# Optimization experiments

Hardware: AMD Instinct MI355X
Metric: run time of the kernel (lower is better)

Reference implementation:

```python
import jax, jax.numpy as jnp
import numpy as np

# ---- static hash-grid config (matches tcnn HashGrid in __init__) ----
L = 16            # n_levels
T = 1 << 19       # hashmap size per level
BASE = 16
MAXR = 4096
GEO = 15
SCALE = np.exp((np.log(MAXR) - np.log(BASE)) / (L - 1))
RES = np.floor(BASE * SCALE ** np.arange(L)).astype(np.int64)  # per-level resolution
PRIMES = np.array([1, 2654435761, 805459861], dtype=np.uint32)
CORNERS = np.array([[(i >> 2) & 1, (i >> 1) & 1, i & 1] for i in range(8)], dtype=np.float32)  # [8,3]


@jax.custom_vjp
def trunc_exp(x):
    return jnp.exp(x)

def _te_fwd(x):
    return jnp.exp(x), x

def _te_bwd(x, g):
    return (g * jnp.exp(jnp.minimum(x, 15.0)),)

trunc_exp.defvjp(_te_fwd, _te_bwd)


def hash_encode(x, tables):
    """Multi-res hash grid. x: [N,3] in [0,1]; tables: [L,T,2] -> [N, 2*L]."""
    x = jnp.clip(x, 0.0, 1.0)
    feats = []
    for l in range(L):  # fixed small loop over levels
        res = float(RES[l])
        pos = x * res                      # [N,3]
        p0 = jnp.floor(pos)
        f = pos - p0                       # trilinear fractions
        idx = (p0[:, None, :] + CORNERS[None]).astype(jnp.uint32)  # [N,8,3]
        h = (idx[..., 0] * PRIMES[0]) ^ (idx[..., 1] * PRIMES[1]) ^ (idx[..., 2] * PRIMES[2])
        h = (h % np.uint32(T)).astype(jnp.int32)                   # [N,8]
        w = jnp.prod(jnp.where(CORNERS[None] > 0, f[:, None, :], 1.0 - f[:, None, :]), axis=-1)  # [N,8]
        feats.append(jnp.sum(tables[l][h] * w[..., None], axis=1))  # [N,2]
    return jnp.concatenate(feats, axis=-1)  # [N,32]


def sh_deg4(d):
    """Spherical harmonics degree 4 (16 comps) on unit directions d: [N,3]."""
    x, y, z = d[..., 0], d[..., 1], d[..., 2]
    x2, y2, z2 = x * x, y * y, z * z
    xy, yz, xz = x * y, y * z, x * z
    return jnp.stack([
        jnp.full_like(x, 0.28209479177387814),
        -0.48860251190291987 * y, 0.48860251190291987 * z, -0.48860251190291987 * x,
        1.0925484305920792 * xy, -1.0925484305920792 * yz,
        0.94617469575755997 * z2 - 0.31539156525252005,
        -1.0925484305920792 * xz, 0.54627421529603959 * (x2 - y2),
        -0.5900435899266435 * y * (3 * x2 - y2), 2.890611442640554 * xy * z,
        -0.4570457994644658 * y * (4 * z2 - x2 - y2),
        0.3731763325901154 * z * (2 * z2 - 3 * x2 - 3 * y2),
        -0.4570457994644658 * x * (4 * z2 - x2 - y2),
        1.445305721320277 * z * (x2 - y2),
        -0.5900435899266435 * x * (x2 - 3 * y2),
    ], axis=-1)


def setup_inputs() -> dict:
    key = jax.random.key(0)
    ks = jax.random.split(key, 12)
    R, N = 8192, 524288
    rays_o = jax.random.uniform(ks[0], (R, 3), minval=-0.4, maxval=0.4, dtype=jnp.float32)
    d = jax.random.normal(ks[1], (R, 3), dtype=jnp.float32)
    rays_d = d / jnp.linalg.norm(d, axis=-1, keepdims=True)
    ray_indices = jnp.sort(jax.random.randint(ks[2], (N,), 0, R)).astype(jnp.int32)
    t_starts = jax.random.uniform(ks[3], (N,), dtype=jnp.float32) * 0.25
    t_ends = t_starts + jax.random.uniform(ks[4], (N,), dtype=jnp.float32) * 0.02 + 1e-3
    hash_tables = jax.random.uniform(ks[5], (L, T, 2), minval=-1e-4, maxval=1e-4, dtype=jnp.float32)
    base_w0 = jax.random.normal(ks[6], (32, 64), dtype=jnp.float32) * (1.0 / np.sqrt(32))
    base_w1 = jax.random.normal(ks[7], (64, 16), dtype=jnp.float32) * (1.0 / np.sqrt(64))
    head_w0 = jax.random.normal(ks[8], (31, 64), dtype=jnp.float32) * (1.0 / np.sqrt(31))
    head_w1 = jax.random.normal(ks[9], (64, 64), dtype=jnp.float32) * (1.0 / np.sqrt(64))
    head_w2 = jax.random.normal(ks[10], (64, 3), dtype=jnp.float32) * (1.0 / np.sqrt(64))
    aabb = jnp.array([-1., -1., -1., 1., 1., 1.], dtype=jnp.float32)
    return dict(t_starts=t_starts, t_ends=t_ends, rays_o=rays_o, rays_d=rays_d,
                ray_indices=ray_indices, hash_tables=hash_tables,
                base_w0=base_w0, base_w1=base_w1,
                head_w0=head_w0, head_w1=head_w1, head_w2=head_w2, aabb=aabb)


def reference(t_starts, t_ends, rays_o, rays_d, ray_indices, hash_tables,
              base_w0, base_w1, head_w0, head_w1, head_w2, aabb):
    n_rays = rays_o.shape[0]
    aabb_min, aabb_max = aabb[:3], aabb[3:]
    # gather per-sample origins/dirs (irregular gather)
    t_origins = rays_o[ray_indices]
    t_dirs = rays_d[ray_indices]
    tmid = (t_starts + t_ends) * 0.5
    positions = t_origins + t_dirs * tmid[:, None]
    # query_density
    xn = (positions - aabb_min) / (aabb_max - aabb_min + 1e-5)
    selector = jnp.all((xn > 0.0) & (xn < 1.0), axis=-1)
    enc = hash_encode(xn, hash_tables)                   # [N,32]
    h = jax.nn.relu(enc @ base_w0) @ base_w1             # [N,16]
    sigmas = trunc_exp(h[:, 0] - 1.0) * selector         # [N]
    embedding = h[:, 1:]                                 # [N,15]
    # query_rgb: dir=(dir+1)/2 then SH enc maps back to [-1,1] => SH(t_dirs)
    hh = jnp.concatenate([sh_deg4(t_dirs), embedding], axis=-1)  # [N,31]
    rgbs = jax.nn.sigmoid(jax.nn.relu(jax.nn.relu(hh @ head_w0) @ head_w1) @ head_w2)  # [N,3]
    # render_weight_from_density: segment-wise exclusive transmittance
    s = sigmas * (t_ends - t_starts)
    excl = jnp.cumsum(s) - s                              # global exclusive cumsum
    offsets = jax.ops.segment_min(excl, ray_indices, num_segments=n_rays)  # value at each segment start
    trans = jnp.exp(-(excl - offsets[ray_indices]))
    alphas = 1.0 - jnp.exp(-s)
    weights = trans * alphas
    # accumulate_along_rays (segment_sum scatter)
    colors = jax.ops.segment_sum(weights[:, None] * rgbs, ray_indices, num_segments=n_rays)
    opacities = jax.ops.segment_sum(weights, ray_indices, num_segments=n_rays)[:, None]
    depths = jax.ops.segment_sum(weights * tmid, ray_indices, num_segments=n_rays)[:, None]
    depths = depths / jnp.maximum(opacities, jnp.finfo(jnp.float32).eps)  # expected_depths
    return colors, opacities, depths
```

## Files before the change

kernel.cpp:

```cpp
#include <hip/hip_runtime.h>
#include <math.h>

#define NLEV 16
#define TBL  (1u << 19)
#define TMASK (TBL - 1u)

typedef _Float16 half2v  __attribute__((ext_vector_type(2)));
typedef _Float16 half4   __attribute__((ext_vector_type(4)));
typedef _Float16 half8   __attribute__((ext_vector_type(8)));
typedef float    floatx4 __attribute__((ext_vector_type(4)));
typedef unsigned int uint2v __attribute__((ext_vector_type(2)));
typedef unsigned int uint4v __attribute__((ext_vector_type(4)));

struct ResParams { float resf[NLEV]; };

__device__ __forceinline__ float sigmoidf(float x) {
    return 1.0f / (1.0f + __expf(-x));
}

__device__ __forceinline__ float2 unpack_h2(unsigned u) {
    union { unsigned u; half2v h; } c; c.u = u;
    return make_float2((float)c.h[0], (float)c.h[1]);
}

__device__ __forceinline__ int swz64(int row, int col) {
    return row * 64 + ((((col >> 3) ^ (row & 7)) << 3) | (col & 7));
}
__device__ __forceinline__ int swz64_blk(int row, int blk) {
    return row * 64 + ((blk ^ (row & 7)) << 3);
}
__device__ __forceinline__ int swz16(int row, int col) {
    return row * 64 + ((((col >> 3) ^ (row & 7)) << 3) | (col & 7));
}
__device__ __forceinline__ int swz16_blk(int row, int blk) {
    return row * 64 + ((blk ^ (row & 7)) << 3);
}

__global__ __launch_bounds__(256) void k_cvt(
    const float* __restrict__ src, _Float16* __restrict__ dst, int n4)
{
    const int i = blockIdx.x * 256 + threadIdx.x;
    if (i >= n4) return;
    const float4 v = ((const float4*)src)[i];
    half4 o; o[0] = (_Float16)v.x; o[1] = (_Float16)v.y;
    o[2] = (_Float16)v.z; o[3] = (_Float16)v.w;
    ((half4*)dst)[i] = o;
}

struct SampPos { float x0, x1, x2; };

__device__ __forceinline__ SampPos load_pos(
    int i, const float* __restrict__ t_starts, const float* __restrict__ t_ends,
    const float* __restrict__ rays_o, const float* __restrict__ rays_d,
    const int* __restrict__ ray_indices,
    float a0, float a1, float a2, float ib0, float ib1, float ib2)
{
    const int   ri = ray_indices[i];
    const float tmid = 0.5f * (t_starts[i] + t_ends[i]);
    const float xn0 = (rays_o[ri*3+0] + rays_d[ri*3+0]*tmid - a0) * ib0;
    const float xn1 = (rays_o[ri*3+1] + rays_d[ri*3+1]*tmid - a1) * ib1;
    const float xn2 = (rays_o[ri*3+2] + rays_d[ri*3+2]*tmid - a2) * ib2;
    SampPos p;
    p.x0 = fminf(fmaxf(xn0, 0.f), 1.f);
    p.x1 = fminf(fmaxf(xn1, 0.f), 1.f);
    p.x2 = fminf(fmaxf(xn2, 0.f), 1.f);
    return p;
}

__global__ __launch_bounds__(256) void k_hash1(
    const float* __restrict__ t_starts, const float* __restrict__ t_ends,
    const float* __restrict__ rays_o,   const float* __restrict__ rays_d,
    const int*   __restrict__ ray_indices,
    const _Float16* __restrict__ tabh,
    const float* __restrict__ aabb,
    _Float16* __restrict__ encG, int n, ResParams rp)
{
    const int i = blockIdx.x * 256 + threadIdx.x;
    if (i >= n) return;

    const float a0 = aabb[0], a1 = aabb[1], a2 = aabb[2];
    const float ib0 = 1.f / (aabb[3] - a0 + 1e-5f);
    const float ib1 = 1.f / (aabb[4] - a1 + 1e-5f);
    const float ib2 = 1.f / (aabb[5] - a2 + 1e-5f);

    const SampPos A = load_pos(i, t_starts, t_ends, rays_o, rays_d, ray_indices,
                               a0, a1, a2, ib0, ib1, ib2);

    union { _Float16 h[32]; uint4v q[4]; } ev;

    #pragma unroll
    for (int l = 0; l < NLEV; ++l) {
        const float resf = rp.resf[l];
        const _Float16* __restrict__ tab = tabh + (size_t)l * (size_t)(TBL * 2u);

        const float p0 = A.x0*resf, p1 = A.x1*resf, p2 = A.x2*resf;
        const float fl0 = floorf(p0), fl1 = floorf(p1), fl2 = floorf(p2);
        const float f0 = p0-fl0, f1 = p1-fl1, f2 = p2-fl2;
        const unsigned i0 = (unsigned)fl0, i1 = (unsigned)fl1, i2 = (unsigned)fl2;
        const unsigned hy0 = i1 * 2654435761u, hy1 = hy0 + 2654435761u;
        const unsigned hz0 = i2 * 805459861u,  hz1 = hz0 + 805459861u;
        const float g0 = 1.f-f0, g1 = 1.f-f1, g2 = 1.f-f2;
        const unsigned ryz[4] = { hy0^hz0, hy0^hz1, hy1^hz0, hy1^hz1 };
        const float    wyz[4] = { g1*g2,   g1*f2,   f1*g2,   f1*f2 };

        unsigned v0[4], v1[4];
        if (!(i0 & 1u)) {
            #pragma unroll
            for (int c = 0; c < 4; ++c) {
                const unsigned lo = (i0 ^ ryz[c]) & TMASK;
                const uint2v p = *(const uint2v*)(tab + (size_t)(lo & ~1u) * 2u);
                const unsigned sw = lo & 1u;
                v0[c] = sw ? p.y : p.x;
                v1[c] = sw ? p.x : p.y;
            }
        } else {
            #pragma unroll
            for (int c = 0; c < 4; ++c) {
                const unsigned lo = (i0        ^ ryz[c]) & TMASK;
                const unsigned hi = ((i0 + 1u) ^ ryz[c]) & TMASK;
                v0[c] = *(const unsigned*)(tab + (size_t)lo * 2u);
                v1[c] = *(const unsigned*)(tab + (size_t)hi * 2u);
            }
        }

        float e0 = 0.f, e1 = 0.f;
        #pragma unroll
        for (int c = 0; c < 4; ++c) {
            const float wlo = g0 * wyz[c], whi = f0 * wyz[c];
            const float2 t0 = unpack_h2(v0[c]), t1 = unpack_h2(v1[c]);
            e0 += wlo * t0.x + whi * t1.x;
            e1 += wlo * t0.y + whi * t1.y;
        }
        ev.h[2*l]   = (_Float16)(e0 * 1024.f);
        ev.h[2*l+1] = (_Float16)(e1 * 1024.f);
    }

    uint4v* dst = (uint4v*)(encG + (size_t)i * 32);
    #pragma unroll
    for (int q = 0; q < 4; ++q) __builtin_nontemporal_store(ev.q[q], dst + q);
}

__global__ __launch_bounds__(256) void k_mlp(
    const float* __restrict__ t_starts, const float* __restrict__ t_ends,
    const float* __restrict__ rays_o,   const float* __restrict__ rays_d,
    const int*   __restrict__ ray_indices,
    const float* __restrict__ bw0,
    const float* __restrict__ bw1,
    const float* __restrict__ hw0,
    const float* __restrict__ hw1,
    const float* __restrict__ hw2,
    const float* __restrict__ aabb,
    const _Float16* __restrict__ encG,
    float4* __restrict__ srgb, int n)
{
    __shared__ _Float16 sT  [4][16 * 72];
    __shared__ _Float16 sSH [256 * 16];
    __shared__ _Float16 sHB [256 * 16];
    __shared__ _Float16 sW0T[64 * 40];
    __shared__ _Float16 sW1T[64 * 64];
    __shared__ _Float16 sBW0T[64 * 32];
    __shared__ _Float16 sBW1T[16 * 64];
    __shared__ float    sDT [256];

    const int t     = threadIdx.x;
    const int gbase = blockIdx.x * 256;

    {
        const int s  = gbase + t;
        const int ri = ray_indices[s];
        const float ts = t_starts[s], te = t_ends[s];
        const float tmid = 0.5f * (ts + te);
        const float ox = rays_o[ri*3+0], oy = rays_o[ri*3+1], oz = rays_o[ri*3+2];
        const float dx = rays_d[ri*3+0], dy = rays_d[ri*3+1], dz = rays_d[ri*3+2];
        const float a0 = aabb[0], a1 = aabb[1], a2c = aabb[2];
        const float b0 = aabb[3], b1 = aabb[4], b2c = aabb[5];
        const float xn0 = (ox + dx*tmid - a0) / (b0 - a0 + 1e-5f);
        const float xn1 = (oy + dy*tmid - a1) / (b1 - a1 + 1e-5f);
        const float xn2 = (oz + dz*tmid - a2c) / (b2c - a2c + 1e-5f);
        const bool sel = (xn0 > 0.f) && (xn0 < 1.f) && (xn1 > 0.f) && (xn1 < 1.f)
                      && (xn2 > 0.f) && (xn2 < 1.f);
        sDT[t] = sel ? (te - ts) : 0.f;

        const float x = dx, y = dy, z = dz;
        const float x2 = x*x, y2 = y*y, z2 = z*z;
        const float xy = x*y, yz = y*z, xz = x*z;
        float shv[16];
        shv[0]  = 0.28209479177387814f;
        shv[1]  = -0.48860251190291987f * y;
        shv[2]  = 0.48860251190291987f * z;
        shv[3]  = -0.48860251190291987f * x;
        shv[4]  = 1.0925484305920792f * xy;
        shv[5]  = -1.0925484305920792f * yz;
        shv[6]  = 0.94617469575756f * z2 - 0.31539156525252005f;
        shv[7]  = -1.0925484305920792f * xz;
        shv[8]  = 0.5462742152960396f * (x2 - y2);
        shv[9]  = -0.5900435899266435f * y * (3.f*x2 - y2);
        shv[10] = 2.890611442640554f * xy * z;
        shv[11] = -0.4570457994644658f * y * (4.f*z2 - x2 - y2);
        shv[12] = 0.3731763325901154f * z * (2.f*z2 - 3.f*x2 - 3.f*y2);
        shv[13] = -0.4570457994644658f * x * (4.f*z2 - x2 - y2);
        shv[14] = 1.445305721320277f * z * (x2 - y2);
        shv[15] = -0.5900435899266435f * x * (x2 - 3.f*y2);
        #pragma unroll
        for (int k4 = 0; k4 < 4; ++k4) {
            half4 p;
            #pragma unroll
            for (int j = 0; j < 4; ++j) p[j] = (_Float16)shv[k4*4 + j];
            *(half4*)&sSH[t*16 + k4*4] = p;
        }
    }
    {
        const int nidx = t & 63, g = t >> 6;
        #pragma unroll
        for (int i2 = 0; i2 < 8; ++i2) {
            const int k = g*8 + i2;
            const float v = (k < 31) ? hw0[k*64 + nidx] : 0.f;
            sW0T[nidx*40 + k] = (_Float16)v;
        }
        #pragma unroll
        for (int i2 = 0; i2 < 16; ++i2) {
            const int k = g*16 + i2;
            sW1T[swz64(nidx, k)] = (_Float16)hw1[k*64 + nidx];
        }
        #pragma unroll
        for (int i2 = 0; i2 < 8; ++i2) {
            const int k = g*8 + i2;
            sBW0T[nidx*32 + k] = (_Float16)bw0[k*64 + nidx];
        }
    }
    {
        const int nidx = t & 15, g = t >> 4;
        #pragma unroll
        for (int i2 = 0; i2 < 4; ++i2) {
            const int k = g*4 + i2;
            sBW1T[swz16(nidx, k)] = (_Float16)bw1[k*16 + nidx];
        }
    }

    const int lane = t & 63, w = t >> 6;
    const int nn = lane & 15, quad = lane >> 4;
    _Float16* myT = &sT[w][0];

    half8 BH2[2];
    #pragma unroll
    for (int ks = 0; ks < 2; ++ks)
        #pragma unroll
        for (int j = 0; j < 8; ++j) {
            const int k = ks*32 + quad*8 + j;
            BH2[ks][j] = (nn < 3) ? (_Float16)hw2[k*3 + nn] : (_Float16)0.f;
        }

    __syncthreads();

    const int rbase = w * 64;

    #pragma unroll
    for (int rt = 0; rt < 4; ++rt) {
        const int srow = rbase + rt*16;
        const int drow = srow + quad*4;

        half8 bE = *(const half8*)(encG + (size_t)(gbase + srow + nn)*32 + quad*8);
        #pragma unroll
        for (int ct = 0; ct < 4; ++ct) {
            half8 aW = *(const half8*)&sBW0T[(ct*16 + nn)*32 + quad*8];
            floatx4 acc = {0.f, 0.f, 0.f, 0.f};
            acc = __builtin_amdgcn_mfma_f32_16x16x32_f16(aW, bE, acc, 0, 0, 0);
            half4 p;
            #pragma unroll
            for (int r2 = 0; r2 < 4; ++r2) p[r2] = (_Float16)fmaxf(acc[r2], 0.f);
            *(half4*)&myT[nn*72 + ct*16 + quad*4] = p;
        }

        float sigr[4];
        {
            half8 a20 = *(const half8*)&myT[nn*72 +  0 + quad*8];
            half8 a21 = *(const half8*)&myT[nn*72 + 32 + quad*8];
            half8 b20 = *(const half8*)&sBW1T[swz16_blk(nn, quad)];
            half8 b21 = *(const half8*)&sBW1T[swz16_blk(nn, 4 + quad)];
            floatx4 acc = {0.f, 0.f, 0.f, 0.f};
            acc = __builtin_amdgcn_mfma_f32_16x16x32_f16(a20, b20, acc, 0, 0, 0);
            acc = __builtin_amdgcn_mfma_f32_16x16x32_f16(a21, b21, acc, 0, 0, 0);
            #pragma unroll
            for (int r2 = 0; r2 < 4; ++r2) {
                const float h = acc[r2] * (1.f / 1024.f);
                const float h0 = __shfl(h, lane & 0x30, 64);
                sigr[r2] = __expf(h0 - 1.f) * sDT[drow + r2];
                if (nn == 0) sHB[(drow + r2)*16 + 15] = (_Float16)0.f;
                else         sHB[(drow + r2)*16 + (nn - 1)] = (_Float16)h;
            }
        }

        half8 shf = *(const half8*)&sSH[(srow + nn)*16 + (quad & 1)*8];
        half8 hbf = *(const half8*)&sHB[(srow + nn)*16 + (quad & 1)*8];
        half8 a3f = (quad < 2) ? shf : hbf;
        #pragma unroll
        for (int ct = 0; ct < 4; ++ct) {
            half8 aW = *(const half8*)&sW0T[(ct*16 + nn)*40 + quad*8];
            floatx4 acc = {0.f, 0.f, 0.f, 0.f};
            acc = __builtin_amdgcn_mfma_f32_16x16x32_f16(aW, a3f, acc, 0, 0, 0);
            half4 p;
            #pragma unroll
            for (int r2 = 0; r2 < 4; ++r2) p[r2] = (_Float16)fmaxf(acc[r2], 0.f);
            *(half4*)&myT[nn*72 + ct*16 + quad*4] = p;
        }

        half8 af0 = *(const half8*)&myT[nn*72 +  0 + quad*8];
        half8 af1 = *(const half8*)&myT[nn*72 + 32 + quad*8];
        #pragma unroll
        for (int ct = 0; ct < 4; ++ct) {
            half8 aW0 = *(const half8*)&sW1T[swz64_blk(ct*16 + nn, quad)];
            half8 aW1 = *(const half8*)&sW1T[swz64_blk(ct*16 + nn, 4 + quad)];
            floatx4 acc = {0.f, 0.f, 0.f, 0.f};
            acc = __builtin_amdgcn_mfma_f32_16x16x32_f16(aW0, af0, acc, 0, 0, 0);
            acc = __builtin_amdgcn_mfma_f32_16x16x32_f16(aW1, af1, acc, 0, 0, 0);
            half4 p;
            #pragma unroll
            for (int r2 = 0; r2 < 4; ++r2) p[r2] = (_Float16)fmaxf(acc[r2], 0.f);
            *(half4*)&myT[nn*72 + ct*16 + quad*4] = p;
        }

        {
            half8 a50 = *(const half8*)&myT[nn*72 +  0 + quad*8];
            half8 a51 = *(const half8*)&myT[nn*72 + 32 + quad*8];
            floatx4 acc = {0.f, 0.f, 0.f, 0.f};
            acc = __builtin_amdgcn_mfma_f32_16x16x32_f16(a50, BH2[0], acc, 0, 0, 0);
            acc = __builtin_amdgcn_mfma_f32_16x16x32_f16(a51, BH2[1], acc, 0, 0, 0);
            #pragma unroll
            for (int r2 = 0; r2 < 4; ++r2) {
                float* bp = (float*)&srgb[gbase + drow + r2];
                if (nn < 3)       bp[1 + nn] = sigmoidf(acc[r2]);
                else if (nn == 3) bp[0]      = sigr[r2];
            }
        }
    }
}

__global__ __launch_bounds__(256) void k_render(
    const float* __restrict__ t_starts, const float* __restrict__ t_ends,
    const int*   __restrict__ ray_indices,
    const float4* __restrict__ srgb,
    float* __restrict__ out, int n_samples, int n_rays)
{
    const int wid  = (blockIdx.x * 256 + threadIdx.x) >> 6;
    const int lane = threadIdx.x & 63;
    if (wid >= n_rays) return;
    const int r = wid;

    int lo = 0, hi = n_samples;
    while (lo < hi) { int mid = (lo + hi) >> 1; if (ray_indices[mid] <  r) lo = mid + 1; else hi = mid; }
    const int start = lo;
    hi = n_samples;
    while (lo < hi) { int mid = (lo + hi) >> 1; if (ray_indices[mid] <= r) lo = mid + 1; else hi = mid; }
    const int end = lo;

    float S = 0.f, cr = 0.f, cg = 0.f, cb = 0.f, op = 0.f, dw = 0.f;
    for (int j0 = start; j0 < end; j0 += 64) {
        const int j = j0 + lane;
        float s = 0.f, R = 0.f, G = 0.f, B = 0.f, tm = 0.f;
        if (j < end) {
            const float4 v = srgb[j];
            s = v.x; R = v.y; G = v.z; B = v.w;
            tm = 0.5f * (t_starts[j] + t_ends[j]);
        }
        float incl = s;
        #pragma unroll
        for (int off = 1; off < 64; off <<= 1) {
            const float tv = __shfl_up(incl, off, 64);
            if (lane >= off) incl += tv;
        }
        const float excl  = incl - s;
        const float trans = __expf(-(S + excl));
        const float alpha = 1.f - __expf(-s);
        const float wgt   = trans * alpha;
        cr += wgt * R; cg += wgt * G; cb += wgt * B;
        op += wgt;     dw += wgt * tm;
        S += __shfl(incl, 63, 64);
    }
    #pragma unroll
    for (int off = 1; off < 64; off <<= 1) {
        cr += __shfl_xor(cr, off, 64);
        cg += __shfl_xor(cg, off, 64);
        cb += __shfl_xor(cb, off, 64);
        op += __shfl_xor(op, off, 64);
        dw += __shfl_xor(dw, off, 64);
    }
    if (lane == 0) {
        out[r*3 + 0] = cr;
        out[r*3 + 1] = cg;
        out[r*3 + 2] = cb;
        out[n_rays*3 + r] = op;
        out[n_rays*4 + r] = dw / fmaxf(op, 1.1920929e-7f);
    }
}

extern "C" void kernel_launch(void* const* d_in, const int* in_sizes, int n_in,
                              void* d_out, int out_size, void* d_ws, size_t ws_size,
                              hipStream_t stream)
{
    const float* t_starts    = (const float*)d_in[0];
    const float* t_ends      = (const float*)d_in[1];
    const float* rays_o      = (const float*)d_in[2];
    const float* rays_d      = (const float*)d_in[3];
    const int*   ray_indices = (const int*)  d_in[4];
    const float* tables      = (const float*)d_in[5];
    const float* bw0         = (const float*)d_in[6];
    const float* bw1         = (const float*)d_in[7];
    const float* hw0         = (const float*)d_in[8];
    const float* hw1         = (const float*)d_in[9];
    const float* hw2         = (const float*)d_in[10];
    const float* aabb        = (const float*)d_in[11];

    const int n      = in_sizes[0];
    const int n_rays = in_sizes[2] / 3;
    const int tbl_n  = in_sizes[5];

    float* out = (float*)d_out;
    char*  ws  = (char*)d_ws;

    const size_t tabh_bytes = (size_t)tbl_n * 2;
    const size_t enc_bytes  = (size_t)n * 64;

    ResParams rp;
    const double scale = exp((log(4096.0) - log(16.0)) / 15.0);
    for (int l = 0; l < NLEV; ++l)
        rp.resf[l] = (float)floor(16.0 * pow(scale, (double)l));

    _Float16* tabh = (_Float16*)ws;
    _Float16* encG = (_Float16*)(ws + tabh_bytes);
    float4*   srgb = (float4*)(ws + tabh_bytes + enc_bytes);

    const int n4 = tbl_n / 4;
    k_cvt<<<(n4 + 255)/256, 256, 0, stream>>>(tables, tabh, n4);

    k_hash1<<<(n + 255)/256, 256, 0, stream>>>(
        t_starts, t_ends, rays_o, rays_d, ray_indices, tabh, aabb, encG, n, rp);

    k_mlp<<<(n + 255)/256, 256, 0, stream>>>(
        t_starts, t_ends, rays_o, rays_d, ray_indices, bw0, bw1, hw0, hw1, hw2,
        aabb, encG, srgb, n);
    k_render<<<(n_rays*64 + 255)/256, 256, 0, stream>>>(
        t_starts, t_ends, ray_indices, srgb, out, n, n_rays);
}
```

Measured before the change: 322.0 us.

## Interleave two MLP row tiles per wave and precompute ray segment bounds

The MLP kernel now processes two 16-row tiles at once, interleaving independent MFMA chains, and stores intermediate activations in a swizzled shared-memory layout instead of padded rows. The intent is to hide MFMA latency and reduce LDS bank conflicts. A new k_bounds kernel, preceded by a memset, records each ray's start and end sample index so the render kernel no longer runs two binary searches per ray. This adds an extra launch and memset, more registers per wave, and an extra workspace buffer placed after srgb.

```diff
diff --git a/kernel.cpp b/kernel.cpp
--- a/kernel.cpp
+++ b/kernel.cpp
@@ -138,6 +138,16 @@
     uint4v* dst = (uint4v*)(encG + (size_t)i * 32);
     #pragma unroll
     for (int q = 0; q < 4; ++q) __builtin_nontemporal_store(ev.q[q], dst + q);
+}
+
+__global__ __launch_bounds__(256) void k_bounds(
+    const int* __restrict__ ray_indices, int* __restrict__ se, int n)
+{
+    const int i = blockIdx.x * 256 + threadIdx.x;
+    if (i >= n) return;
+    const int r = ray_indices[i];
+    if (i == 0 || ray_indices[i-1] != r) se[2*r]     = i;
+    if (i == n-1 || ray_indices[i+1] != r) se[2*r+1] = i + 1;
 }
 
 __global__ __launch_bounds__(256) void k_mlp(
@@ -153,7 +163,7 @@
     const _Float16* __restrict__ encG,
     float4* __restrict__ srgb, int n)
 {
-    __shared__ _Float16 sT  [4][16 * 72];
+    __shared__ _Float16 sT  [4][2048];
     __shared__ _Float16 sSH [256 * 16];
     __shared__ _Float16 sHB [256 * 16];
     __shared__ _Float16 sW0T[64 * 40];
@@ -239,7 +249,8 @@
 
     const int lane = t & 63, w = t >> 6;
     const int nn = lane & 15, quad = lane >> 4;
-    _Float16* myT = &sT[w][0];
+    _Float16* T0 = &sT[w][0];
+    _Float16* T1 = &sT[w][1024];
 
     half8 BH2[2];
     #pragma unroll
@@ -255,81 +266,127 @@
     const int rbase = w * 64;
 
     #pragma unroll
-    for (int rt = 0; rt < 4; ++rt) {
-        const int srow = rbase + rt*16;
-        const int drow = srow + quad*4;
-
-        half8 bE = *(const half8*)(encG + (size_t)(gbase + srow + nn)*32 + quad*8);
+    for (int p = 0; p < 2; ++p) {
+        const int s0 = rbase + p*32;
+        const int s1 = s0 + 16;
+        const int d0 = s0 + quad*4;
+        const int d1 = s1 + quad*4;
+
+        half8 bE0 = *(const half8*)(encG + (size_t)(gbase + s0 + nn)*32 + quad*8);
+        half8 bE1 = *(const half8*)(encG + (size_t)(gbase + s1 + nn)*32 + quad*8);
         #pragma unroll
         for (int ct = 0; ct < 4; ++ct) {
             half8 aW = *(const half8*)&sBW0T[(ct*16 + nn)*32 + quad*8];
-            floatx4 acc = {0.f, 0.f, 0.f, 0.f};
-            acc = __builtin_amdgcn_mfma_f32_16x16x32_f16(aW, bE, acc, 0, 0, 0);
-            half4 p;
-            #pragma unroll
-            for (int r2 = 0; r2 < 4; ++r2) p[r2] = (_Float16)fmaxf(acc[r2], 0.f);
-            *(half4*)&myT[nn*72 + ct*16 + quad*4] = p;
-        }
-
-        float sigr[4];
+            floatx4 a0 = {0.f,0.f,0.f,0.f}, a1 = {0.f,0.f,0.f,0.f};
+            a0 = __builtin_amdgcn_mfma_f32_16x16x32_f16(aW, bE0, a0, 0, 0, 0);
+            a1 = __builtin_amdgcn_mfma_f32_16x16x32_f16(aW, bE1, a1, 0, 0, 0);
+            half4 p0, p1;
+            #pragma unroll
+            for (int r2 = 0; r2 < 4; ++r2) {
+                p0[r2] = (_Float16)fmaxf(a0[r2], 0.f);
+                p1[r2] = (_Float16)fmaxf(a1[r2], 0.f);
+            }
+            *(half4*)&T0[swz16(nn, ct*16 + quad*4)] = p0;
+            *(half4*)&T1[swz16(nn, ct*16 + quad*4)] = p1;
+        }
+
+        float sig0[4], sig1[4];
         {
-            half8 a20 = *(const half8*)&myT[nn*72 +  0 + quad*8];
-            half8 a21 = *(const half8*)&myT[nn*72 + 32 + quad*8];
             half8 b20 = *(const half8*)&sBW1T[swz16_blk(nn, quad)];
             half8 b21 = *(const half8*)&sBW1T[swz16_blk(nn, 4 + quad)];
-            floatx4 acc = {0.f, 0.f, 0.f, 0.f};
-            acc = __builtin_amdgcn_mfma_f32_16x16x32_f16(a20, b20, acc, 0, 0, 0);
-            acc = __builtin_amdgcn_mfma_f32_16x16x32_f16(a21, b21, acc, 0, 0, 0);
+            half8 a200 = *(const half8*)&T0[swz16_blk(nn, quad)];
+            half8 a201 = *(const half8*)&T0[swz16_blk(nn, 4 + quad)];
+            half8 a210 = *(const half8*)&T1[swz16_blk(nn, quad)];
+            half8 a211 = *(const half8*)&T1[swz16_blk(nn, 4 + quad)];
+            floatx4 c0 = {0.f,0.f,0.f,0.f}, c1 = {0.f,0.f,0.f,0.f};
+            c0 = __builtin_amdgcn_mfma_f32_16x16x32_f16(a200, b20, c0, 0, 0, 0);
+            c1 = __builtin_amdgcn_mfma_f32_16x16x32_f16(a210, b20, c1, 0, 0, 0);
+            c0 = __builtin_amdgcn_mfma_f32_16x16x32_f16(a201, b21, c0, 0, 0, 0);
+            c1 = __builtin_amdgcn_mfma_f32_16x16x32_f16(a211, b21, c1, 0, 0, 0);
             #pragma unroll
             for (int r2 = 0; r2 < 4; ++r2) {
-                const float h = acc[r2] * (1.f / 1024.f);
-                const float h0 = __shfl(h, lane & 0x30, 64);
-                sigr[r2] = __expf(h0 - 1.f) * sDT[drow + r2];
-                if (nn == 0) sHB[(drow + r2)*16 + 15] = (_Float16)0.f;
-                else         sHB[(drow + r2)*16 + (nn - 1)] = (_Float16)h;
-            }
-        }
-
-        half8 shf = *(const half8*)&sSH[(srow + nn)*16 + (quad & 1)*8];
-        half8 hbf = *(const half8*)&sHB[(srow + nn)*16 + (quad & 1)*8];
-        half8 a3f = (quad < 2) ? shf : hbf;
+                const float h0v = c0[r2] * (1.f / 1024.f);
+                const float h1v = c1[r2] * (1.f / 1024.f);
+                const float b0v = __shfl(h0v, lane & 0x30, 64);
+                const float b1v = __shfl(h1v, lane & 0x30, 64);
+                sig0[r2] = __expf(b0v - 1.f) * sDT[d0 + r2];
+                sig1[r2] = __expf(b1v - 1.f) * sDT[d1 + r2];
+                if (nn == 0) {
+                    sHB[(d0 + r2)*16 + 15] = (_Float16)0.f;
+                    sHB[(d1 + r2)*16 + 15] = (_Float16)0.f;
+                } else {
+                    sHB[(d0 + r2)*16 + (nn - 1)] = (_Float16)h0v;
+                    sHB[(d1 + r2)*16 + (nn - 1)] = (_Float16)h1v;
+                }
+            }
+        }
+
+        half8 sh0 = *(const half8*)&sSH[(s0 + nn)*16 + (quad & 1)*8];
+        half8 hb0 = *(const half8*)&sHB[(s0 + nn)*16 + (quad & 1)*8];
+        half8 sh1 = *(const half8*)&sSH[(s1 + nn)*16 + (quad & 1)*8];
+        half8 hb1 = *(const half8*)&sHB[(s1 + nn)*16 + (quad & 1)*8];
+        half8 f30 = (quad < 2) ? sh0 : hb0;
+        half8 f31 = (quad < 2) ? sh1 : hb1;
         #pragma unroll
         for (int ct = 0; ct < 4; ++ct) {
             half8 aW = *(const half8*)&sW0T[(ct*16 + nn)*40 + quad*8];
-            floatx4 acc = {0.f, 0.f, 0.f, 0.f};
-            acc = __builtin_amdgcn_mfma_f32_16x16x32_f16(aW, a3f, acc, 0, 0, 0);
-            half4 p;
-            #pragma unroll
-            for (int r2 = 0; r2 < 4; ++r2) p[r2] = (_Float16)fmaxf(acc[r2], 0.f);
-            *(half4*)&myT[nn*72 + ct*16 + quad*4] = p;
-        }
-
-        half8 af0 = *(const half8*)&myT[nn*72 +  0 + quad*8];
-        half8 af1 = *(const half8*)&myT[nn*72 + 32 + quad*8];
+            floatx4 a0 = {0.f,0.f,0.f,0.f}, a1 = {0.f,0.f,0.f,0.f};
+            a0 = __builtin_amdgcn_mfma_f32_16x16x32_f16(aW, f30, a0, 0, 0, 0);
+            a1 = __builtin_amdgcn_mfma_f32_16x16x32_f16(aW, f31, a1, 0, 0, 0);
+            half4 p0, p1;
+            #pragma unroll
+            for (int r2 = 0; r2 < 4; ++r2) {
+                p0[r2] = (_Float16)fmaxf(a0[r2], 0.f);
+                p1[r2] = (_Float16)fmaxf(a1[r2], 0.f);
+            }
+            *(half4*)&T0[swz16(nn, ct*16 + quad*4)] = p0;
+            *(half4*)&T1[swz16(nn, ct*16 + quad*4)] = p1;
+        }
+
+        half8 af00 = *(const half8*)&T0[swz16_blk(nn, quad)];
+        half8 af01 = *(const half8*)&T0[swz16_blk(nn, 4 + quad)];
+        half8 af10 = *(const half8*)&T1[swz16_blk(nn, quad)];
+        half8 af11 = *(const half8*)&T1[swz16_blk(nn, 4 + quad)];
         #pragma unroll
         for (int ct = 0; ct < 4; ++ct) {
             half8 aW0 = *(const half8*)&sW1T[swz64_blk(ct*16 + nn, quad)];
             half8 aW1 = *(const half8*)&sW1T[swz64_blk(ct*16 + nn, 4 + quad)];
-            floatx4 acc = {0.f, 0.f, 0.f, 0.f};
-            acc = __builtin_amdgcn_mfma_f32_16x16x32_f16(aW0, af0, acc, 0, 0, 0);
-            acc = __builtin_amdgcn_mfma_f32_16x16x32_f16(aW1, af1, acc, 0, 0, 0);
-            half4 p;
-            #pragma unroll
-            for (int r2 = 0; r2 < 4; ++r2) p[r2] = (_Float16)fmaxf(acc[r2], 0.f);
-            *(half4*)&myT[nn*72 + ct*16 + quad*4] = p;
+            floatx4 a0 = {0.f,0.f,0.f,0.f}, a1 = {0.f,0.f,0.f,0.f};
+            a0 = __builtin_amdgcn_mfma_f32_16x16x32_f16(aW0, af00, a0, 0, 0, 0);
+            a1 = __builtin_amdgcn_mfma_f32_16x16x32_f16(aW0, af10, a1, 0, 0, 0);
+            a0 = __builtin_amdgcn_mfma_f32_16x16x32_f16(aW1, af01, a0, 0, 0, 0);
+            a1 = __builtin_amdgcn_mfma_f32_16x16x32_f16(aW1, af11, a1, 0, 0, 0);
+            half4 p0, p1;
+            #pragma unroll
+            for (int r2 = 0; r2 < 4; ++r2) {
+                p0[r2] = (_Float16)fmaxf(a0[r2], 0.f);
+                p1[r2] = (_Float16)fmaxf(a1[r2], 0.f);
+            }
+            *(half4*)&T0[swz16(nn, ct*16 + quad*4)] = p0;
+            *(half4*)&T1[swz16(nn, ct*16 + quad*4)] = p1;
         }
 
         {
-            half8 a50 = *(const half8*)&myT[nn*72 +  0 + quad*8];
-            half8 a51 = *(const half8*)&myT[nn*72 + 32 + quad*8];
-            floatx4 acc = {0.f, 0.f, 0.f, 0.f};
-            acc = __builtin_amdgcn_mfma_f32_16x16x32_f16(a50, BH2[0], acc, 0, 0, 0);
-            acc = __builtin_amdgcn_mfma_f32_16x16x32_f16(a51, BH2[1], acc, 0, 0, 0);
+            half8 a500 = *(const half8*)&T0[swz16_blk(nn, quad)];
+            half8 a501 = *(const half8*)&T0[swz16_blk(nn, 4 + quad)];
+            half8 a510 = *(const half8*)&T1[swz16_blk(nn, quad)];
+            half8 a511 = *(const half8*)&T1[swz16_blk(nn, 4 + quad)];
+            floatx4 c0 = {0.f,0.f,0.f,0.f}, c1 = {0.f,0.f,0.f,0.f};
+            c0 = __builtin_amdgcn_mfma_f32_16x16x32_f16(a500, BH2[0], c0, 0, 0, 0);
+            c1 = __builtin_amdgcn_mfma_f32_16x16x32_f16(a510, BH2[0], c1, 0, 0, 0);
+            c0 = __builtin_amdgcn_mfma_f32_16x16x32_f16(a501, BH2[1], c0, 0, 0, 0);
+            c1 = __builtin_amdgcn_mfma_f32_16x16x32_f16(a511, BH2[1], c1, 0, 0, 0);
             #pragma unroll
             for (int r2 = 0; r2 < 4; ++r2) {
-                float* bp = (float*)&srgb[gbase + drow + r2];
-                if (nn < 3)       bp[1 + nn] = sigmoidf(acc[r2]);
-                else if (nn == 3) bp[0]      = sigr[r2];
+                float* bp0 = (float*)&srgb[gbase + d0 + r2];
+                float* bp1 = (float*)&srgb[gbase + d1 + r2];
+                if (nn < 3) {
+                    bp0[1 + nn] = sigmoidf(c0[r2]);
+                    bp1[1 + nn] = sigmoidf(c1[r2]);
+                } else if (nn == 3) {
+                    bp0[0] = sig0[r2];
+                    bp1[0] = sig1[r2];
+                }
             }
         }
     }
@@ -337,21 +394,17 @@
 
 __global__ __launch_bounds__(256) void k_render(
     const float* __restrict__ t_starts, const float* __restrict__ t_ends,
-    const int*   __restrict__ ray_indices,
+    const int*   __restrict__ se,
     const float4* __restrict__ srgb,
-    float* __restrict__ out, int n_samples, int n_rays)
+    float* __restrict__ out, int n_rays)
 {
     const int wid  = (blockIdx.x * 256 + threadIdx.x) >> 6;
     const int lane = threadIdx.x & 63;
     if (wid >= n_rays) return;
     const int r = wid;
 
-    int lo = 0, hi = n_samples;
-    while (lo < hi) { int mid = (lo + hi) >> 1; if (ray_indices[mid] <  r) lo = mid + 1; else hi = mid; }
-    const int start = lo;
-    hi = n_samples;
-    while (lo < hi) { int mid = (lo + hi) >> 1; if (ray_indices[mid] <= r) lo = mid + 1; else hi = mid; }
-    const int end = lo;
+    const int start = se[2*r];
+    const int end   = se[2*r + 1];
 
     float S = 0.f, cr = 0.f, cg = 0.f, cb = 0.f, op = 0.f, dw = 0.f;
     for (int j0 = start; j0 < end; j0 += 64) {
@@ -419,6 +472,7 @@
 
     const size_t tabh_bytes = (size_t)tbl_n * 2;
     const size_t enc_bytes  = (size_t)n * 64;
+    const size_t srgb_bytes = (size_t)n * 16;
 
     ResParams rp;
     const double scale = exp((log(4096.0) - log(16.0)) / 15.0);
@@ -428,9 +482,13 @@
     _Float16* tabh = (_Float16*)ws;
     _Float16* encG = (_Float16*)(ws + tabh_bytes);
     float4*   srgb = (float4*)(ws + tabh_bytes + enc_bytes);
+    int*      se   = (int*)(ws + tabh_bytes + enc_bytes + srgb_bytes);
 
     const int n4 = tbl_n / 4;
     k_cvt<<<(n4 + 255)/256, 256, 0, stream>>>(tables, tabh, n4);
+
+    hipMemsetAsync(se, 0, (size_t)n_rays * 2 * sizeof(int), stream);
+    k_bounds<<<(n + 255)/256, 256, 0, stream>>>(ray_indices, se, n);
 
     k_hash1<<<(n + 255)/256, 256, 0, stream>>>(
         t_starts, t_ends, rays_o, rays_d, ray_indices, tabh, aabb, encG, n, rp);
@@ -438,6 +496,7 @@
     k_mlp<<<(n + 255)/256, 256, 0, stream>>>(
         t_starts, t_ends, rays_o, rays_d, ray_indices, bw0, bw1, hw0, hw1, hw2,
         aabb, encG, srgb, n);
+
     k_render<<<(n_rays*64 + 255)/256, 256, 0, stream>>>(
-        t_starts, t_ends, ray_indices, srgb, out, n, n_rays);
-}
+        t_starts, t_ends, se, srgb, out, n_rays);
+}
```

Result: faster. 312.9 us (-2.8%).
